# Optimization experiments

Measured on AMD Instinct MI355X. Metric: run time of the kernel, lower is better.

Reference implementation:

```python
import jax, jax.numpy as jnp
import numpy as np

N = 100000
E = 1000000
IN_DIM = 64
OUT_DIM = 64


def setup_inputs() -> dict:
    key = jax.random.key(0)
    k1, k2, k3, k4 = jax.random.split(key, 4)
    x = jax.random.normal(k1, (N, IN_DIM), dtype=jnp.float32)
    edge_index = jax.random.randint(k2, (2, E), 0, N, dtype=jnp.int64)
    # nn.Linear(in_dim, out_dim): weight (out,in), bias (out,)
    bound = 1.0 / np.sqrt(IN_DIM)
    W = jax.random.uniform(k3, (OUT_DIM, IN_DIM), dtype=jnp.float32, minval=-bound, maxval=bound)
    b = jax.random.uniform(k4, (OUT_DIM,), dtype=jnp.float32, minval=-bound, maxval=bound)
    return {"x": x, "edge_index": edge_index, "W": W, "b": b}


def reference(x, edge_index, W, b):
    i = edge_index[0]  # target nodes (E,)
    j = edge_index[1]  # source nodes (E,)
    msg = x[j] @ W.T + b  # (E, out_dim)
    n = x.shape[0]
    out = jax.ops.segment_sum(msg, i, num_segments=n)  # (N, out_dim)
    deg = jax.ops.segment_sum(jnp.ones((i.shape[0],), dtype=msg.dtype), i, num_segments=n)
    deg = jnp.maximum(deg, 1.0)[:, None]
    return out / deg
```

## Files before the change

kernel.cpp:

```cpp
#include <hip/hip_runtime.h>

constexpr int N_NODES = 100000;
constexpr int N_EDGES = 1000000;
constexpr int DIM = 64;

constexpr int BNODES = 256;
constexpr int NBUCK  = (N_NODES + BNODES - 1) / BNODES;
constexpr int SCAP   = 3584;
constexpr int CHUNK  = 2048;
constexpr int NWG_A  = (N_EDGES + CHUNK - 1) / CHUNK;

constexpr int CAP  = 16;
constexpr int MAXO = 32768;

constexpr int TILE = 64;
constexpr int PAD  = 65;

__global__ __launch_bounds__(256) void bin_edges(
    const int* __restrict__ eidx, int* __restrict__ gcur,
    int* __restrict__ staging)
{
    __shared__ int hist[NBUCK];
    __shared__ int gbase[NBUCK];
    __shared__ int cur[NBUCK];

    const int tid = threadIdx.x;
    const int e0  = blockIdx.x * CHUNK;
    const int n   = (N_EDGES - e0 < CHUNK) ? (N_EDGES - e0) : CHUNK;

    for (int t = tid; t < NBUCK; t += 256) hist[t] = 0;
    __syncthreads();

    for (int t = tid; t < n; t += 256) {
        int i = eidx[e0 + t];
        atomicAdd(&hist[i >> 8], 1);
    }
    __syncthreads();

    for (int t = tid; t < NBUCK; t += 256) {
        int c = hist[t];
        gbase[t] = (c > 0) ? atomicAdd(&gcur[t], c) : 0;
        cur[t] = 0;
    }
    __syncthreads();

    for (int t = tid; t < n; t += 256) {
        int i  = eidx[e0 + t];
        int j  = eidx[N_EDGES + e0 + t];
        int bk = i >> 8;
        int pos = atomicAdd(&cur[bk], 1);
        int dst = gbase[bk] + pos;
        if (dst < SCAP)
            staging[bk * SCAP + dst] = ((i & 255) << 17) | j;
    }
}

__global__ __launch_bounds__(256) void fused_gather_mm(
    const float* __restrict__ x, const int* __restrict__ gcur,
    const int* __restrict__ staging,
    const float* __restrict__ W, const float* __restrict__ b,
    int* __restrict__ noflow, int* __restrict__ oflow,
    int* __restrict__ deg_g, float* __restrict__ out)
{
    __shared__ float tile[TILE * PAD];
    __shared__ int   lds_slot[TILE * CAP];
    __shared__ int   lcnt[TILE];

    const int tid  = threadIdx.x;
    const int base = blockIdx.x * TILE;
    const int bk   = blockIdx.x >> 2;
    const int sub  = blockIdx.x & 3;

    if (tid < TILE) lcnt[tid] = 0;
    __syncthreads();

    int m = gcur[bk];
    if (m > SCAP) m = SCAP;
    const int sg = bk * SCAP;
    for (int t = tid; t < m; t += 256) {
        int pk  = staging[sg + t];
        int off = pk >> 17;
        if ((off >> 6) == sub) {
            int r = off & 63;
            int pos = atomicAdd(&lcnt[r], 1);
            if (pos < CAP) {
                lds_slot[(r << 4) + pos] = pk & 0x1FFFF;
            } else {
                int o = atomicAdd(noflow, 1);
                if (o < MAXO) {
                    oflow[2 * o]     = (bk << 8) + off;
                    oflow[2 * o + 1] = pk & 0x1FFFF;
                }
            }
        }
    }
    __syncthreads();

    if (tid < TILE) {
        int g = base + tid;
        if (g < N_NODES) deg_g[g] = lcnt[tid];
    }

    const int lane = tid & 63;
    const int wid  = tid >> 6;
    const int grp  = lane >> 4;
    const int l16  = lane & 15;
    const int c4   = l16 << 2;

#pragma unroll
    for (int pack = 0; pack < 4; ++pack) {
        const int row    = wid * 16 + pack * 4 + grp;
        const int d_true = lcnt[row];
        const int d      = (d_true < CAP) ? d_true : CAP;

        int jv[16];
#pragma unroll
        for (int u = 0; u < 16; ++u) jv[u] = lds_slot[(row << 4) + u];

        float4 vb[16];
#pragma unroll
        for (int u = 0; u < 16; ++u) {
            const int jj = (u < d) ? jv[u] : 0;
            vb[u] = *reinterpret_cast<const float4*>(x + ((size_t)jj << 6) + c4);
        }

        float sx = 0.0f, sy = 0.0f, sz = 0.0f, sw = 0.0f;
#pragma unroll
        for (int u = 0; u < 16; ++u) {
            const bool ok = (u < d);
            sx += ok ? vb[u].x : 0.0f;
            sy += ok ? vb[u].y : 0.0f;
            sz += ok ? vb[u].z : 0.0f;
            sw += ok ? vb[u].w : 0.0f;
        }

        const float inv = (d_true > 0) ? 1.0f / (float)d_true : 0.0f;
        const int tb = row * PAD + c4;
        tile[tb + 0] = sx * inv;
        tile[tb + 1] = sy * inv;
        tile[tb + 2] = sz * inv;
        tile[tb + 3] = sw * inv;
    }
    __syncthreads();

    const int nd  = tid & 63;
    const int d0u = __builtin_amdgcn_readfirstlane((tid >> 6) << 4);
    const float* __restrict__ Wr = W + (size_t)d0u * DIM;

    float acc[16];
#pragma unroll
    for (int q = 0; q < 16; ++q) acc[q] = 0.0f;

#pragma unroll 4
    for (int k = 0; k < DIM; ++k) {
        float a = tile[nd * PAD + k];
#pragma unroll
        for (int q = 0; q < 16; ++q)
            acc[q] = fmaf(a, Wr[(size_t)q * DIM + k], acc[q]);
    }

    const int dg = lcnt[nd];
    __syncthreads();
#pragma unroll
    for (int q = 0; q < 16; ++q) {
        float v = (dg > 0) ? (acc[q] + b[d0u + q]) : 0.0f;
        tile[nd * PAD + d0u + q] = v;
    }
    __syncthreads();

#pragma unroll
    for (int r = 0; r < 16; ++r) {
        int idx = r * 256 + tid;
        int row = idx >> 6, d = idx & 63;
        int g = base + row;
        if (g < N_NODES)
            out[(size_t)g * DIM + d] = tile[row * PAD + d];
    }
}

__global__ __launch_bounds__(256) void fixup_overflow(
    const int* __restrict__ noflow, const int* __restrict__ oflow,
    const int* __restrict__ deg_g, const float* __restrict__ x,
    const float* __restrict__ W, float* __restrict__ out)
{
    int m = *noflow;
    if (m > MAXO) m = MAXO;
    const int lane = threadIdx.x & 63;
    const int wv   = (blockIdx.x * 256 + threadIdx.x) >> 6;
    const int nwv  = (gridDim.x * 256) >> 6;
    const float* __restrict__ wr = W + ((size_t)lane << 6);
    for (int o = wv; o < m; o += nwv) {
        const int i = oflow[2 * o];
        const int j = oflow[2 * o + 1];
        const float inv = 1.0f / (float)deg_g[i];
        const float* __restrict__ xr = x + ((size_t)j << 6);
        float acc = 0.0f;
#pragma unroll
        for (int k4 = 0; k4 < 16; ++k4) {
            const float4 xv  = *reinterpret_cast<const float4*>(xr + 4 * k4);
            const float4 wv4 = *reinterpret_cast<const float4*>(wr + 4 * k4);
            acc = fmaf(xv.x, wv4.x, acc);
            acc = fmaf(xv.y, wv4.y, acc);
            acc = fmaf(xv.z, wv4.z, acc);
            acc = fmaf(xv.w, wv4.w, acc);
        }
        atomicAdd(&out[((size_t)i << 6) + lane], acc * inv);
    }
}

extern "C" void kernel_launch(void* const* d_in, const int* in_sizes, int n_in,
                              void* d_out, int out_size, void* d_ws, size_t ws_size,
                              hipStream_t stream) {
    const float* x  = (const float*)d_in[0];
    const int*   ei = (const int*)d_in[1];
    const float* W  = (const float*)d_in[2];
    const float* b  = (const float*)d_in[3];
    float* out = (float*)d_out;

    int* gcur    = (int*)d_ws;
    int* noflow  = gcur + NBUCK;
    int* oflow   = noflow + 1;
    int* deg_g   = oflow + 2 * MAXO;
    int* staging = deg_g + N_NODES;

    hipMemsetAsync(gcur, 0, (NBUCK + 1) * sizeof(int), stream);

    bin_edges<<<NWG_A, 256, 0, stream>>>(ei, gcur, staging);
    fused_gather_mm<<<(N_NODES + TILE - 1) / TILE, 256, 0, stream>>>(
        x, gcur, staging, W, b, noflow, oflow, deg_g, out);
    fixup_overflow<<<128, 256, 0, stream>>>(noflow, oflow, deg_g, x, W, out);
}
```

Before: 200.9 us.

## Bin edges with direct global atomics into sub-partitioned staging buckets

The chunked LDS-histogram binning pass is replaced by a one-edge-per-thread kernel. Each thread takes a slot with a global atomic on one of 8 sub-counters per bucket, chosen by block index to spread contention. The gather kernel then walks the 8 sub-regions of its bucket, and a sched_barrier is added after the x-row loads so the loads stay grouped ahead of the accumulation. This removes the three-phase LDS histogram and its barriers, at the cost of about 1M contended global atomics. Edges that overflow a sub-bucket are written to the overflow list but never counted in the degree, so the result would be wrong if overflow ever occurred.

```diff
diff --git a/kernel.cpp b/kernel.cpp
--- a/kernel.cpp
+++ b/kernel.cpp
@@ -6,9 +6,9 @@
 
 constexpr int BNODES = 256;
 constexpr int NBUCK  = (N_NODES + BNODES - 1) / BNODES;
-constexpr int SCAP   = 3584;
-constexpr int CHUNK  = 2048;
-constexpr int NWG_A  = (N_EDGES + CHUNK - 1) / CHUNK;
+constexpr int NSUB   = 8;
+constexpr int SUBCAP = 448;
+constexpr int SCAP   = NSUB * SUBCAP;
 
 constexpr int CAP  = 16;
 constexpr int MAXO = 32768;
@@ -18,40 +18,20 @@
 
 __global__ __launch_bounds__(256) void bin_edges(
     const int* __restrict__ eidx, int* __restrict__ gcur,
-    int* __restrict__ staging)
+    int* __restrict__ staging, int* __restrict__ noflow, int* __restrict__ oflow)
 {
-    __shared__ int hist[NBUCK];
-    __shared__ int gbase[NBUCK];
-    __shared__ int cur[NBUCK];
-
-    const int tid = threadIdx.x;
-    const int e0  = blockIdx.x * CHUNK;
-    const int n   = (N_EDGES - e0 < CHUNK) ? (N_EDGES - e0) : CHUNK;
-
-    for (int t = tid; t < NBUCK; t += 256) hist[t] = 0;
-    __syncthreads();
-
-    for (int t = tid; t < n; t += 256) {
-        int i = eidx[e0 + t];
-        atomicAdd(&hist[i >> 8], 1);
-    }
-    __syncthreads();
-
-    for (int t = tid; t < NBUCK; t += 256) {
-        int c = hist[t];
-        gbase[t] = (c > 0) ? atomicAdd(&gcur[t], c) : 0;
-        cur[t] = 0;
-    }
-    __syncthreads();
-
-    for (int t = tid; t < n; t += 256) {
-        int i  = eidx[e0 + t];
-        int j  = eidx[N_EDGES + e0 + t];
-        int bk = i >> 8;
-        int pos = atomicAdd(&cur[bk], 1);
-        int dst = gbase[bk] + pos;
-        if (dst < SCAP)
-            staging[bk * SCAP + dst] = ((i & 255) << 17) | j;
+    int e = blockIdx.x * 256 + threadIdx.x;
+    if (e >= N_EDGES) return;
+    int i  = eidx[e];
+    int j  = eidx[N_EDGES + e];
+    int bk = i >> 8;
+    int s  = blockIdx.x & (NSUB - 1);
+    int pos = atomicAdd(&gcur[s * NBUCK + bk], 1);
+    if (pos < SUBCAP) {
+        staging[bk * SCAP + s * SUBCAP + pos] = ((i & 255) << 17) | j;
+    } else {
+        int o = atomicAdd(noflow, 1);
+        if (o < MAXO) { oflow[2 * o] = i; oflow[2 * o + 1] = j; }
     }
 }
 
@@ -74,22 +54,24 @@
     if (tid < TILE) lcnt[tid] = 0;
     __syncthreads();
 
-    int m = gcur[bk];
-    if (m > SCAP) m = SCAP;
-    const int sg = bk * SCAP;
-    for (int t = tid; t < m; t += 256) {
-        int pk  = staging[sg + t];
-        int off = pk >> 17;
-        if ((off >> 6) == sub) {
-            int r = off & 63;
-            int pos = atomicAdd(&lcnt[r], 1);
-            if (pos < CAP) {
-                lds_slot[(r << 4) + pos] = pk & 0x1FFFF;
-            } else {
-                int o = atomicAdd(noflow, 1);
-                if (o < MAXO) {
-                    oflow[2 * o]     = (bk << 8) + off;
-                    oflow[2 * o + 1] = pk & 0x1FFFF;
+    for (int ss = 0; ss < NSUB; ++ss) {
+        int m = gcur[ss * NBUCK + bk];
+        if (m > SUBCAP) m = SUBCAP;
+        const int sg = bk * SCAP + ss * SUBCAP;
+        for (int t = tid; t < m; t += 256) {
+            int pk  = staging[sg + t];
+            int off = pk >> 17;
+            if ((off >> 6) == sub) {
+                int r = off & 63;
+                int pos = atomicAdd(&lcnt[r], 1);
+                if (pos < CAP) {
+                    lds_slot[(r << 4) + pos] = pk & 0x1FFFF;
+                } else {
+                    int o = atomicAdd(noflow, 1);
+                    if (o < MAXO) {
+                        oflow[2 * o]     = (bk << 8) + off;
+                        oflow[2 * o + 1] = pk & 0x1FFFF;
+                    }
                 }
             }
         }
@@ -123,6 +105,7 @@
             const int jj = (u < d) ? jv[u] : 0;
             vb[u] = *reinterpret_cast<const float4*>(x + ((size_t)jj << 6) + c4);
         }
+        __builtin_amdgcn_sched_barrier(0);
 
         float sx = 0.0f, sy = 0.0f, sz = 0.0f, sw = 0.0f;
 #pragma unroll
@@ -218,14 +201,15 @@
     float* out = (float*)d_out;
 
     int* gcur    = (int*)d_ws;
-    int* noflow  = gcur + NBUCK;
+    int* noflow  = gcur + NSUB * NBUCK;
     int* oflow   = noflow + 1;
     int* deg_g   = oflow + 2 * MAXO;
     int* staging = deg_g + N_NODES;
 
-    hipMemsetAsync(gcur, 0, (NBUCK + 1) * sizeof(int), stream);
-
-    bin_edges<<<NWG_A, 256, 0, stream>>>(ei, gcur, staging);
+    hipMemsetAsync(gcur, 0, (NSUB * NBUCK + 1) * sizeof(int), stream);
+
+    bin_edges<<<(N_EDGES + 255) / 256, 256, 0, stream>>>(
+        ei, gcur, staging, noflow, oflow);
     fused_gather_mm<<<(N_NODES + TILE - 1) / TILE, 256, 0, stream>>>(
         x, gcur, staging, W, b, noflow, oflow, deg_g, out);
     fixup_overflow<<<128, 256, 0, stream>>>(noflow, oflow, deg_g, x, W, out);
```

Result: slower. 277.0 us (+37.9%).

## Split slot building into separate kernel and simplify bin_edges to single pass

Applied to the files above, without the earlier changes.

bin_edges now loads each edge once into registers and reuses the shared-memory histogram atomic's return value as the rank, dropping the second read and the second atomic pass. A new slotify kernel handles each 256-node bucket once and writes per-node slot lists and degrees to global memory, so the gather kernel no longer scans the staging bucket four times. The gather kernel now reads slots with coalesced int4 loads and gathers one float per lane per row. The cost is an extra launch and a global round-trip for the slot array, and SCAP and MAXO are smaller, which raises the risk of dropping edges if a bucket or the overflow list fills up.

```diff
diff --git a/kernel.cpp b/kernel.cpp
--- a/kernel.cpp
+++ b/kernel.cpp
@@ -6,12 +6,13 @@
 
 constexpr int BNODES = 256;
 constexpr int NBUCK  = (N_NODES + BNODES - 1) / BNODES;
-constexpr int SCAP   = 3584;
+constexpr int SCAP   = 3072;
 constexpr int CHUNK  = 2048;
+constexpr int EPT    = 8;
 constexpr int NWG_A  = (N_EDGES + CHUNK - 1) / CHUNK;
 
 constexpr int CAP  = 16;
-constexpr int MAXO = 32768;
+constexpr int MAXO = 16384;
 
 constexpr int TILE = 64;
 constexpr int PAD  = 65;
@@ -22,56 +23,56 @@
 {
     __shared__ int hist[NBUCK];
     __shared__ int gbase[NBUCK];
-    __shared__ int cur[NBUCK];
 
     const int tid = threadIdx.x;
     const int e0  = blockIdx.x * CHUNK;
-    const int n   = (N_EDGES - e0 < CHUNK) ? (N_EDGES - e0) : CHUNK;
 
     for (int t = tid; t < NBUCK; t += 256) hist[t] = 0;
-    __syncthreads();
-
-    for (int t = tid; t < n; t += 256) {
-        int i = eidx[e0 + t];
-        atomicAdd(&hist[i >> 8], 1);
-    }
+
+    int iv[EPT], jv[EPT], rk[EPT];
+#pragma unroll
+    for (int u = 0; u < EPT; ++u) {
+        int e = e0 + u * 256 + tid;
+        bool ok = (e < N_EDGES);
+        iv[u] = ok ? eidx[e] : -1;
+        jv[u] = ok ? eidx[N_EDGES + e] : 0;
+    }
+    __syncthreads();
+
+#pragma unroll
+    for (int u = 0; u < EPT; ++u)
+        if (iv[u] >= 0) rk[u] = atomicAdd(&hist[iv[u] >> 8], 1);
     __syncthreads();
 
     for (int t = tid; t < NBUCK; t += 256) {
         int c = hist[t];
         gbase[t] = (c > 0) ? atomicAdd(&gcur[t], c) : 0;
-        cur[t] = 0;
-    }
-    __syncthreads();
-
-    for (int t = tid; t < n; t += 256) {
-        int i  = eidx[e0 + t];
-        int j  = eidx[N_EDGES + e0 + t];
-        int bk = i >> 8;
-        int pos = atomicAdd(&cur[bk], 1);
-        int dst = gbase[bk] + pos;
-        if (dst < SCAP)
-            staging[bk * SCAP + dst] = ((i & 255) << 17) | j;
-    }
-}
-
-__global__ __launch_bounds__(256) void fused_gather_mm(
-    const float* __restrict__ x, const int* __restrict__ gcur,
-    const int* __restrict__ staging,
-    const float* __restrict__ W, const float* __restrict__ b,
+    }
+    __syncthreads();
+
+#pragma unroll
+    for (int u = 0; u < EPT; ++u) {
+        if (iv[u] >= 0) {
+            int bk  = iv[u] >> 8;
+            int dst = gbase[bk] + rk[u];
+            if (dst < SCAP)
+                staging[bk * SCAP + dst] = ((iv[u] & 255) << 17) | jv[u];
+        }
+    }
+}
+
+__global__ __launch_bounds__(256) void slotify(
+    const int* __restrict__ gcur, const int* __restrict__ staging,
     int* __restrict__ noflow, int* __restrict__ oflow,
-    int* __restrict__ deg_g, float* __restrict__ out)
-{
-    __shared__ float tile[TILE * PAD];
-    __shared__ int   lds_slot[TILE * CAP];
-    __shared__ int   lcnt[TILE];
-
-    const int tid  = threadIdx.x;
-    const int base = blockIdx.x * TILE;
-    const int bk   = blockIdx.x >> 2;
-    const int sub  = blockIdx.x & 3;
-
-    if (tid < TILE) lcnt[tid] = 0;
+    int* __restrict__ deg_g, int* __restrict__ slot_g)
+{
+    __shared__ int lcnt[BNODES];
+    __shared__ int lsl[BNODES * CAP];
+
+    const int tid = threadIdx.x;
+    const int bk  = blockIdx.x;
+
+    lcnt[tid] = 0;
     __syncthreads();
 
     int m = gcur[bk];
@@ -80,66 +81,74 @@
     for (int t = tid; t < m; t += 256) {
         int pk  = staging[sg + t];
         int off = pk >> 17;
-        if ((off >> 6) == sub) {
-            int r = off & 63;
-            int pos = atomicAdd(&lcnt[r], 1);
-            if (pos < CAP) {
-                lds_slot[(r << 4) + pos] = pk & 0x1FFFF;
-            } else {
-                int o = atomicAdd(noflow, 1);
-                if (o < MAXO) {
-                    oflow[2 * o]     = (bk << 8) + off;
-                    oflow[2 * o + 1] = pk & 0x1FFFF;
-                }
+        int pos = atomicAdd(&lcnt[off], 1);
+        if (pos < CAP) {
+            lsl[(off << 4) + pos] = pk & 0x1FFFF;
+        } else {
+            int o = atomicAdd(noflow, 1);
+            if (o < MAXO) {
+                oflow[2 * o]     = (bk << 8) + off;
+                oflow[2 * o + 1] = pk & 0x1FFFF;
             }
         }
     }
     __syncthreads();
 
-    if (tid < TILE) {
-        int g = base + tid;
-        if (g < N_NODES) deg_g[g] = lcnt[tid];
-    }
-
+    const int node = (bk << 8) + tid;
+    if (node < N_NODES) {
+        deg_g[node] = lcnt[tid];
+        int4* dst = reinterpret_cast<int4*>(slot_g + ((size_t)node << 4));
+        const int4* src = reinterpret_cast<const int4*>(lsl + (tid << 4));
+        dst[0] = src[0]; dst[1] = src[1]; dst[2] = src[2]; dst[3] = src[3];
+    }
+}
+
+__global__ __launch_bounds__(256) void fused_gather_mm(
+    const float* __restrict__ x, const int* __restrict__ deg_g,
+    const int* __restrict__ slot_g,
+    const float* __restrict__ W, const float* __restrict__ b,
+    float* __restrict__ out)
+{
+    __shared__ float tile[TILE * PAD];
+    __shared__ int   lslot[TILE * CAP];
+    __shared__ int   ldeg[TILE];
+
+    const int tid  = threadIdx.x;
+    const int base = blockIdx.x * TILE;
     const int lane = tid & 63;
     const int wid  = tid >> 6;
-    const int grp  = lane >> 4;
-    const int l16  = lane & 15;
-    const int c4   = l16 << 2;
-
-#pragma unroll
-    for (int pack = 0; pack < 4; ++pack) {
-        const int row    = wid * 16 + pack * 4 + grp;
-        const int d_true = lcnt[row];
-        const int d      = (d_true < CAP) ? d_true : CAP;
-
-        int jv[16];
-#pragma unroll
-        for (int u = 0; u < 16; ++u) jv[u] = lds_slot[(row << 4) + u];
-
-        float4 vb[16];
+
+    {
+        const int4 v = *reinterpret_cast<const int4*>(
+            slot_g + ((size_t)base << 4) + (tid << 2));
+        *reinterpret_cast<int4*>(lslot + (tid << 2)) = v;
+        if (tid < TILE) {
+            int g = base + tid;
+            ldeg[tid] = (g < N_NODES) ? deg_g[g] : 0;
+        }
+    }
+    __syncthreads();
+
+    for (int i = 0; i < 16; ++i) {
+        const int row    = wid * 16 + i;
+        const int d_true = ldeg[row];
+        const int dd     = (d_true < CAP) ? d_true : CAP;
+
+        float v[16];
 #pragma unroll
         for (int u = 0; u < 16; ++u) {
-            const int jj = (u < d) ? jv[u] : 0;
-            vb[u] = *reinterpret_cast<const float4*>(x + ((size_t)jj << 6) + c4);
-        }
-
-        float sx = 0.0f, sy = 0.0f, sz = 0.0f, sw = 0.0f;
-#pragma unroll
-        for (int u = 0; u < 16; ++u) {
-            const bool ok = (u < d);
-            sx += ok ? vb[u].x : 0.0f;
-            sy += ok ? vb[u].y : 0.0f;
-            sz += ok ? vb[u].z : 0.0f;
-            sw += ok ? vb[u].w : 0.0f;
-        }
+            const int ju = lslot[(row << 4) + u];
+            const int jj = (u < dd) ? ju : 0;
+            v[u] = x[((size_t)jj << 6) + lane];
+        }
+
+        float s = 0.0f;
+#pragma unroll
+        for (int u = 0; u < 16; ++u)
+            s += (u < dd) ? v[u] : 0.0f;
 
         const float inv = (d_true > 0) ? 1.0f / (float)d_true : 0.0f;
-        const int tb = row * PAD + c4;
-        tile[tb + 0] = sx * inv;
-        tile[tb + 1] = sy * inv;
-        tile[tb + 2] = sz * inv;
-        tile[tb + 3] = sw * inv;
+        tile[row * PAD + lane] = s * inv;
     }
     __syncthreads();
 
@@ -159,12 +168,12 @@
             acc[q] = fmaf(a, Wr[(size_t)q * DIM + k], acc[q]);
     }
 
-    const int dg = lcnt[nd];
+    const int dg = ldeg[nd];
     __syncthreads();
 #pragma unroll
     for (int q = 0; q < 16; ++q) {
-        float v = (dg > 0) ? (acc[q] + b[d0u + q]) : 0.0f;
-        tile[nd * PAD + d0u + q] = v;
+        float v2 = (dg > 0) ? (acc[q] + b[d0u + q]) : 0.0f;
+        tile[nd * PAD + d0u + q] = v2;
     }
     __syncthreads();
 
@@ -221,12 +230,14 @@
     int* noflow  = gcur + NBUCK;
     int* oflow   = noflow + 1;
     int* deg_g   = oflow + 2 * MAXO;
-    int* staging = deg_g + N_NODES;
+    int* slot_g  = deg_g + N_NODES;
+    int* staging = slot_g + N_NODES * 16 + 1024;
 
     hipMemsetAsync(gcur, 0, (NBUCK + 1) * sizeof(int), stream);
 
     bin_edges<<<NWG_A, 256, 0, stream>>>(ei, gcur, staging);
+    slotify<<<NBUCK, 256, 0, stream>>>(gcur, staging, noflow, oflow, deg_g, slot_g);
     fused_gather_mm<<<(N_NODES + TILE - 1) / TILE, 256, 0, stream>>>(
-        x, gcur, staging, W, b, noflow, oflow, deg_g, out);
+        x, deg_g, slot_g, W, b, out);
     fixup_overflow<<<128, 256, 0, stream>>>(noflow, oflow, deg_g, x, W, out);
 }
```

Result: no change. 201.2 us (+0.1%).
